# Kernel tuning notes

Measured on AMD Instinct MI355X. Metric: run time of the kernel, lower is better.

The kernel has to match this reference:

```python
import jax, jax.numpy as jnp
import numpy as np

N_NODES = 100000
N_EDGES = 3200000
N_GRAPHS = 64


def gcn_conv(x, W, b, src, dst, n_nodes):
    # PyG GCNConv: add self-loops, symmetric degree normalization, then
    # out[dst] += norm * (x @ W)[src], plus bias.
    h = x @ W  # [N, out]
    loop = jnp.arange(n_nodes)
    s = jnp.concatenate([src, loop])
    d = jnp.concatenate([dst, loop])
    deg = jax.ops.segment_sum(jnp.ones_like(d, dtype=h.dtype), d, num_segments=n_nodes)
    dinv = jnp.where(deg > 0, jax.lax.rsqrt(deg), 0.0)
    norm = dinv[s] * dinv[d]  # [E+N]
    msg = norm[:, None] * h[s]  # gather + scale
    out = jax.ops.segment_sum(msg, d, num_segments=n_nodes)  # scatter-add
    return out + b


def global_mean_pool(x, batch, num_graphs):
    sums = jax.ops.segment_sum(x, batch, num_segments=num_graphs)
    cnts = jax.ops.segment_sum(jnp.ones((x.shape[0],), x.dtype), batch, num_segments=num_graphs)
    return sums / jnp.maximum(cnts, 1.0)[:, None]


def setup_inputs() -> dict:
    key = jax.random.key(0)
    ks = jax.random.split(key, 12)
    x = jax.random.normal(ks[0], (N_NODES, 128), dtype=jnp.float32)
    edge_index = jax.random.randint(ks[1], (2, N_EDGES), 0, N_NODES, dtype=jnp.int64 if jax.config.jax_enable_x64 else jnp.int32)
    batch = jnp.sort(jax.random.randint(ks[2], (N_NODES,), 0, N_GRAPHS))
    def lin(k, fan_in, fan_out):
        bound = 1.0 / np.sqrt(fan_in)
        kw, kb = jax.random.split(k)
        W = jax.random.uniform(kw, (fan_in, fan_out), minval=-bound, maxval=bound, dtype=jnp.float32)
        b = jax.random.uniform(kb, (fan_out,), minval=-bound, maxval=bound, dtype=jnp.float32)
        return W, b
    W1, b1 = lin(ks[3], 128, 16)
    W2, b2 = lin(ks[4], 16, 32)
    Wf1, bf1 = lin(ks[5], 32, 64)
    Wf2, bf2 = lin(ks[6], 64, 8)
    return {"x": x, "edge_index": edge_index, "batch": batch,
            "W1": W1, "b1": b1, "W2": W2, "b2": b2,
            "Wf1": Wf1, "bf1": bf1, "Wf2": Wf2, "bf2": bf2}


def reference(x, edge_index, batch, W1, b1, W2, b2, Wf1, bf1, Wf2, bf2):
    src, dst = edge_index[0], edge_index[1]
    n = x.shape[0]
    h = jax.nn.relu(gcn_conv(x, W1, b1, src, dst, n))
    h = jax.nn.relu(gcn_conv(h, W2, b2, src, dst, n))
    g = global_mean_pool(h, batch, N_GRAPHS)  # [G, 32]
    g = jax.nn.relu(g @ Wf1 + bf1)
    return g @ Wf2 + bf2  # [G, num_actions]
```

## Files before the change

### kernel.cpp

```cpp
#include <hip/hip_runtime.h>
#include <hip/hip_fp16.h>

#define N_NODES  100000
#define N_EDGES  3200000
#define N_GRAPHS 64

#define BSHIFT   7
#define BMASK    127
#define NBUCK    782
#define CAP      4608
#define PB_BLK   1000
#define PB_CHUNK 3200
#define PB_CH4   800

#define SCALE1   2097152.0f
#define ISCALE1  (1.0f / 2097152.0f)
#define SCALE2   1048576.0f
#define ISCALE2  (1.0f / 1048576.0f)
#define SCALEP   65536.0f
#define ISCALEP  (1.0f / 65536.0f)


#define EDGEACC(p_, r_, SC) { \
    int d_ = (int)((p_) >> 17); \
    float2 f01_ = __half22float2(*(const __half2*)&(r_).x); \
    float2 f23_ = __half22float2(*(const __half2*)&(r_).y); \
    int* a_ = &acc[d_ * 17 + f4 * 4]; \
    atomicAdd(a_ + 0, __float2int_rn(f01_.x * (SC))); \
    atomicAdd(a_ + 1, __float2int_rn(f01_.y * (SC))); \
    atomicAdd(a_ + 2, __float2int_rn(f23_.x * (SC))); \
    atomicAdd(a_ + 3, __float2int_rn(f23_.y * (SC))); }

#define LOADR(k_, w_, P_) uint2 r##k_ = *(const uint2*)((P_) + ((w_) & 0x1FFFF) * 16 + f4 * 4);

__global__ void __launch_bounds__(256) hist_pass(const int* __restrict__ dst,
                                                 unsigned int* __restrict__ histG) {
    __shared__ int hist[NBUCK];
    int t = threadIdx.x;
    const int4* d4p = (const int4*)(dst + blockIdx.x * PB_CHUNK);
    for (int i = t; i < NBUCK; i += 256) hist[i] = 0;
    __syncthreads();
    int i = t;
    for (; i + 256 < PB_CH4; i += 512) {
        int4 a = d4p[i];
        int4 b = d4p[i + 256];
        atomicAdd(&hist[a.x >> BSHIFT], 1); atomicAdd(&hist[a.y >> BSHIFT], 1);
        atomicAdd(&hist[a.z >> BSHIFT], 1); atomicAdd(&hist[a.w >> BSHIFT], 1);
        atomicAdd(&hist[b.x >> BSHIFT], 1); atomicAdd(&hist[b.y >> BSHIFT], 1);
        atomicAdd(&hist[b.z >> BSHIFT], 1); atomicAdd(&hist[b.w >> BSHIFT], 1);
    }
    for (; i < PB_CH4; i += 256) {
        int4 a = d4p[i];
        atomicAdd(&hist[a.x >> BSHIFT], 1); atomicAdd(&hist[a.y >> BSHIFT], 1);
        atomicAdd(&hist[a.z >> BSHIFT], 1); atomicAdd(&hist[a.w >> BSHIFT], 1);
    }
    __syncthreads();
    for (int i2 = t; i2 < NBUCK; i2 += 256)
        histG[blockIdx.x * NBUCK + i2] = (unsigned int)hist[i2];
}

__global__ void __launch_bounds__(256) scan_pass(const unsigned int* __restrict__ histG,
                                                 unsigned int* __restrict__ baseG,
                                                 int* __restrict__ cntG) {
    __shared__ unsigned int s[256];
    int b = blockIdx.x, t = threadIdx.x;
    unsigned int v0 = (t * 4 + 0 < PB_BLK) ? histG[(t * 4 + 0) * NBUCK + b] : 0;
    unsigned int v1 = (t * 4 + 1 < PB_BLK) ? histG[(t * 4 + 1) * NBUCK + b] : 0;
    unsigned int v2 = (t * 4 + 2 < PB_BLK) ? histG[(t * 4 + 2) * NBUCK + b] : 0;
    unsigned int v3 = (t * 4 + 3 < PB_BLK) ? histG[(t * 4 + 3) * NBUCK + b] : 0;
    unsigned int tot = v0 + v1 + v2 + v3;
    s[t] = tot;
    __syncthreads();
    for (int o = 1; o < 256; o <<= 1) {
        unsigned int x = (t >= o) ? s[t - o] : 0;
        __syncthreads();
        s[t] += x;
        __syncthreads();
    }
    unsigned int ex = s[t] - tot;
    unsigned int base = (unsigned int)b * CAP + ex;
    if (t * 4 + 0 < PB_BLK) baseG[b * PB_BLK + t * 4 + 0] = base;
    if (t * 4 + 1 < PB_BLK) baseG[b * PB_BLK + t * 4 + 1] = base + v0;
    if (t * 4 + 2 < PB_BLK) baseG[b * PB_BLK + t * 4 + 2] = base + v0 + v1;
    if (t * 4 + 3 < PB_BLK) baseG[b * PB_BLK + t * 4 + 3] = base + v0 + v1 + v2;
    if (t == 255) cntG[b] = (int)(ex + tot);
}

#define PLACE1(d_, s_) { \
    int bb_ = (d_) >> BSHIFT; \
    unsigned int pk_ = ((unsigned int)((d_) & BMASK) << 17) | (unsigned int)(s_); \
    int slot_ = atomicAdd(&cur[bb_], 1); \
    st[slot_] = pk_; bkt[slot_] = (unsigned short)bb_; }

__global__ void __launch_bounds__(256) place_pass(const int* __restrict__ src,
                                                  const int* __restrict__ dst,
                                                  const unsigned int* __restrict__ histG,
                                                  const unsigned int* __restrict__ baseG,
                                                  unsigned int* __restrict__ stage) {
    __shared__ int off[NBUCK];
    __shared__ int cur[NBUCK];
    __shared__ unsigned int gbase[NBUCK];
    __shared__ int part[256];
    __shared__ unsigned int st[PB_CHUNK];
    __shared__ unsigned short bkt[PB_CHUNK];
    int t = threadIdx.x, blk = blockIdx.x;

    int b4 = t * 4;
    int h0 = (b4 + 0 < NBUCK) ? (int)histG[blk * NBUCK + b4 + 0] : 0;
    int h1 = (b4 + 1 < NBUCK) ? (int)histG[blk * NBUCK + b4 + 1] : 0;
    int h2 = (b4 + 2 < NBUCK) ? (int)histG[blk * NBUCK + b4 + 2] : 0;
    int h3 = (b4 + 3 < NBUCK) ? (int)histG[blk * NBUCK + b4 + 3] : 0;
    int tot = h0 + h1 + h2 + h3;
    part[t] = tot;
    __syncthreads();
    for (int o = 1; o < 256; o <<= 1) {
        int v = (t >= o) ? part[t - o] : 0;
        __syncthreads();
        part[t] += v;
        __syncthreads();
    }
    int ex = part[t] - tot;
    if (b4 + 0 < NBUCK) { off[b4 + 0] = ex;                cur[b4 + 0] = ex; }
    if (b4 + 1 < NBUCK) { off[b4 + 1] = ex + h0;           cur[b4 + 1] = ex + h0; }
    if (b4 + 2 < NBUCK) { off[b4 + 2] = ex + h0 + h1;      cur[b4 + 2] = ex + h0 + h1; }
    if (b4 + 3 < NBUCK) { off[b4 + 3] = ex + h0 + h1 + h2; cur[b4 + 3] = ex + h0 + h1 + h2; }
    for (int i = t; i < NBUCK; i += 256) gbase[i] = baseG[i * PB_BLK + blk];
    __syncthreads();

    const int4* d4p = (const int4*)(dst + blk * PB_CHUNK);
    const int4* s4p = (const int4*)(src + blk * PB_CHUNK);
    int i = t;
    for (; i + 256 < PB_CH4; i += 512) {
        int4 d0 = d4p[i],        s0 = s4p[i];
        int4 d1_ = d4p[i + 256], s1_ = s4p[i + 256];
        PLACE1(d0.x, s0.x); PLACE1(d0.y, s0.y); PLACE1(d0.z, s0.z); PLACE1(d0.w, s0.w);
        PLACE1(d1_.x, s1_.x); PLACE1(d1_.y, s1_.y); PLACE1(d1_.z, s1_.z); PLACE1(d1_.w, s1_.w);
    }
    for (; i < PB_CH4; i += 256) {
        int4 d0 = d4p[i], s0 = s4p[i];
        PLACE1(d0.x, s0.x); PLACE1(d0.y, s0.y); PLACE1(d0.z, s0.z); PLACE1(d0.w, s0.w);
    }
    __syncthreads();

    for (int i2 = t; i2 < PB_CHUNK; i2 += 256) {
        int b = bkt[i2];
        unsigned int gs = gbase[b] + (unsigned int)(i2 - off[b]);
        if (gs < (unsigned int)(b + 1) * CAP) stage[gs] = st[i2];
    }
}

__global__ void __launch_bounds__(256) bucket_dinv(const unsigned int* __restrict__ stage,
                                                   const int* __restrict__ cntG,
                                                   float* __restrict__ dinv) {
    __shared__ int ldeg[128];
    int b = blockIdx.x, t = threadIdx.x;
    int base = b * CAP;
    int cnt = cntG[b]; if (cnt > CAP) cnt = CAP;
    if (t < 128) ldeg[t] = 0;
    __syncthreads();
    int i0 = t * 4;
    for (; i0 + 4 <= cnt; i0 += 1024) {
        uint4 p = *(const uint4*)(stage + base + i0);
        atomicAdd(&ldeg[p.x >> 17], 1);
        atomicAdd(&ldeg[p.y >> 17], 1);
        atomicAdd(&ldeg[p.z >> 17], 1);
        atomicAdd(&ldeg[p.w >> 17], 1);
    }
    for (int j = i0; j < cnt && j < i0 + 4; j++)
        atomicAdd(&ldeg[stage[base + j] >> 17], 1);
    __syncthreads();
    int v = b * 128 + t;
    if (t < 128 && v < N_NODES) dinv[v] = rsqrtf((float)(ldeg[t] + 1));
}

#define MM1_ROWS 64
__global__ void __launch_bounds__(256) mm1(const float* __restrict__ x,
                                           const float* __restrict__ W,
                                           const float* __restrict__ dinv,
                                           __half* __restrict__ hs) {
    __shared__ float ws[128 * 16];
    __shared__ float xs[MM1_ROWS * 132];
    int t = threadIdx.x;
    int row0 = blockIdx.x * MM1_ROWS;
    for (int i = t; i < 2048; i += 256) ws[i] = W[i];
    for (int i = t; i < 2048; i += 256) {
        int r = i >> 5, c4 = (i & 31) * 4;
        int v = row0 + r;
        float4 val = (v < N_NODES) ? *(const float4*)(x + (size_t)v * 128 + c4)
                                   : make_float4(0.f, 0.f, 0.f, 0.f);
        *(float4*)&xs[r * 132 + c4] = val;
    }
    __syncthreads();
    int row = t >> 2, c4 = (t & 3) * 4;
    int v = row0 + row;
    if (v < N_NODES) {
        float dv = dinv[v];
        float a0 = 0.f, a1 = 0.f, a2 = 0.f, a3 = 0.f;
#pragma unroll
        for (int k = 0; k < 128; k++) {
            float xv = xs[row * 132 + k];
            float4 w4 = *(const float4*)&ws[k * 16 + c4];
            a0 += xv * w4.x; a1 += xv * w4.y; a2 += xv * w4.z; a3 += xv * w4.w;
        }
        __half2 h01 = __floats2half2_rn(a0 * dv, a1 * dv);
        __half2 h23 = __floats2half2_rn(a2 * dv, a3 * dv);
        uint2 o = make_uint2(*(unsigned*)&h01, *(unsigned*)&h23);
        *(uint2*)(hs + (size_t)v * 16 + c4) = o;
    }
}

__global__ void __launch_bounds__(256) gather1(const unsigned int* __restrict__ stage,
                                               const int* __restrict__ cntG,
                                               const __half* __restrict__ hs,
                                               const float* __restrict__ dinv,
                                               const float* __restrict__ b1,
                                               __half* __restrict__ d1) {
    __shared__ int acc[128 * 17];
    int b = blockIdx.x, t = threadIdx.x;
    int base = b * CAP;
    int cnt = cntG[b]; if (cnt > CAP) cnt = CAP;
    for (int i = t; i < 128 * 17; i += 256) acc[i] = 0;
    __syncthreads();
    int f4 = t & 3;
    int q = t >> 2;
    int i0 = q * 16;
    for (; i0 + 16 <= cnt; i0 += 1024) {
        const uint4* sp = (const uint4*)(stage + base + i0);
        uint4 pa = sp[0], pb = sp[1], pc = sp[2], pd = sp[3];
        LOADR(0,  pa.x, hs) LOADR(1,  pa.y, hs) LOADR(2,  pa.z, hs) LOADR(3,  pa.w, hs)
        LOADR(4,  pb.x, hs) LOADR(5,  pb.y, hs) LOADR(6,  pb.z, hs) LOADR(7,  pb.w, hs)
        LOADR(8,  pc.x, hs) LOADR(9,  pc.y, hs) LOADR(10, pc.z, hs) LOADR(11, pc.w, hs)
        LOADR(12, pd.x, hs) LOADR(13, pd.y, hs) LOADR(14, pd.z, hs) LOADR(15, pd.w, hs)
        EDGEACC(pa.x, r0,  SCALE1) EDGEACC(pa.y, r1,  SCALE1)
        EDGEACC(pa.z, r2,  SCALE1) EDGEACC(pa.w, r3,  SCALE1)
        EDGEACC(pb.x, r4,  SCALE1) EDGEACC(pb.y, r5,  SCALE1)
        EDGEACC(pb.z, r6,  SCALE1) EDGEACC(pb.w, r7,  SCALE1)
        EDGEACC(pc.x, r8,  SCALE1) EDGEACC(pc.y, r9,  SCALE1)
        EDGEACC(pc.z, r10, SCALE1) EDGEACC(pc.w, r11, SCALE1)
        EDGEACC(pd.x, r12, SCALE1) EDGEACC(pd.y, r13, SCALE1)
        EDGEACC(pd.z, r14, SCALE1) EDGEACC(pd.w, r15, SCALE1)
    }
    for (int j = i0; j < cnt && j < i0 + 16; j++) {
        unsigned int p = stage[base + j];
        uint2 r = *(const uint2*)(hs + (p & 0x1FFFF) * 16 + f4 * 4);
        EDGEACC(p, r, SCALE1);
    }
    __syncthreads();
    for (int i = t; i < 512; i += 256) {
        int n = i >> 2, kq = (i & 3) * 4, v = b * 128 + n;
        if (v < N_NODES) {
            float dv = dinv[v];
            const int* ar = &acc[n * 17 + kq];
            uint2 sh = *(const uint2*)(hs + (size_t)v * 16 + kq);
            float2 s01 = __half22float2(*(const __half2*)&sh.x);
            float2 s23 = __half22float2(*(const __half2*)&sh.y);
            float r0 = dv * ((float)ar[0] * ISCALE1 + s01.x) + b1[kq + 0];
            float r1 = dv * ((float)ar[1] * ISCALE1 + s01.y) + b1[kq + 1];
            float r2 = dv * ((float)ar[2] * ISCALE1 + s23.x) + b1[kq + 2];
            float r3 = dv * ((float)ar[3] * ISCALE1 + s23.y) + b1[kq + 3];
            __half2 h01 = __floats2half2_rn(r0 > 0.f ? dv * r0 : 0.f,
                                            r1 > 0.f ? dv * r1 : 0.f);
            __half2 h23 = __floats2half2_rn(r2 > 0.f ? dv * r2 : 0.f,
                                            r3 > 0.f ? dv * r3 : 0.f);
            uint2 o = make_uint2(*(unsigned*)&h01, *(unsigned*)&h23);
            *(uint2*)(d1 + (size_t)v * 16 + kq) = o;
        }
    }
}

__global__ void __launch_bounds__(256) gather2(const unsigned int* __restrict__ stage,
                                               const int* __restrict__ cntG,
                                               const __half* __restrict__ d1,
                                               const float* __restrict__ dinv,
                                               const float* __restrict__ W2,
                                               const float* __restrict__ b2,
                                               const int* __restrict__ batch,
                                               float* __restrict__ gsum,
                                               float* __restrict__ gcnt) {
    __shared__ int acc[128 * 17];
    __shared__ float wl[512];
    __shared__ int lsum[N_GRAPHS * 32];
    __shared__ int lcnt[N_GRAPHS];
    __shared__ int lbat[128];
    float* accf = (float*)acc;
    int b = blockIdx.x, t = threadIdx.x;
    int base = b * CAP;
    int cnt = cntG[b]; if (cnt > CAP) cnt = CAP;
    for (int i = t; i < 128 * 17; i += 256) acc[i] = 0;
    for (int i = t; i < 512; i += 256) wl[i] = W2[i];
    for (int i = t; i < N_GRAPHS * 32; i += 256) lsum[i] = 0;
    if (t < N_GRAPHS) lcnt[t] = 0;
    if (t < 128) {
        int v = b * 128 + t;
        lbat[t] = (v < N_NODES) ? batch[v] : 0;
    }
    __syncthreads();
    int f4 = t & 3;
    int q = t >> 2;
    int i0 = q * 16;
    for (; i0 + 16 <= cnt; i0 += 1024) {
        const uint4* sp = (const uint4*)(stage + base + i0);
        uint4 pa = sp[0], pb = sp[1], pc = sp[2], pd = sp[3];
        LOADR(0,  pa.x, d1) LOADR(1,  pa.y, d1) LOADR(2,  pa.z, d1) LOADR(3,  pa.w, d1)
        LOADR(4,  pb.x, d1) LOADR(5,  pb.y, d1) LOADR(6,  pb.z, d1) LOADR(7,  pb.w, d1)
        LOADR(8,  pc.x, d1) LOADR(9,  pc.y, d1) LOADR(10, pc.z, d1) LOADR(11, pc.w, d1)
        LOADR(12, pd.x, d1) LOADR(13, pd.y, d1) LOADR(14, pd.z, d1) LOADR(15, pd.w, d1)
        EDGEACC(pa.x, r0,  SCALE2) EDGEACC(pa.y, r1,  SCALE2)
        EDGEACC(pa.z, r2,  SCALE2) EDGEACC(pa.w, r3,  SCALE2)
        EDGEACC(pb.x, r4,  SCALE2) EDGEACC(pb.y, r5,  SCALE2)
        EDGEACC(pb.z, r6,  SCALE2) EDGEACC(pb.w, r7,  SCALE2)
        EDGEACC(pc.x, r8,  SCALE2) EDGEACC(pc.y, r9,  SCALE2)
        EDGEACC(pc.z, r10, SCALE2) EDGEACC(pc.w, r11, SCALE2)
        EDGEACC(pd.x, r12, SCALE2) EDGEACC(pd.y, r13, SCALE2)
        EDGEACC(pd.z, r14, SCALE2) EDGEACC(pd.w, r15, SCALE2)
    }
    for (int j = i0; j < cnt && j < i0 + 16; j++) {
        unsigned int p = stage[base + j];
        uint2 r = *(const uint2*)(d1 + (p & 0x1FFFF) * 16 + f4 * 4);
        EDGEACC(p, r, SCALE2);
    }
    __syncthreads();
    for (int i = t; i < 2048; i += 256) {
        int n = i >> 4, k = i & 15, v = b * 128 + n;
        float sum = (float)acc[n * 17 + k] * ISCALE2;
        if (v < N_NODES) sum += __half2float(d1[v * 16 + k]);
        accf[n * 17 + k] = sum;
    }
    __syncthreads();
    int k = t & 31, l0 = t >> 5;
    for (int g = 0; g < 16; g++) {
        int n = l0 + g * 8, v = b * 128 + n;
        if (v < N_NODES) {
            const float* ar = &accf[n * 17];
            float a = 0.f;
#pragma unroll
            for (int j = 0; j < 16; j++) a += ar[j] * wl[j * 32 + k];
            float r = dinv[v] * a + b2[k];
            r = r > 0.f ? r : 0.f;
            int gg = lbat[n];
            atomicAdd(&lsum[gg * 32 + k], __float2int_rn(r * SCALEP));
            if (k == 0) atomicAdd(&lcnt[gg], 1);
        }
    }
    __syncthreads();
    int last = 127; if (b * 128 + last > N_NODES - 1) last = N_NODES - 1 - b * 128;
    int gmin = lbat[0], gmax = lbat[last];
    int ng = gmax - gmin + 1;
    for (int i = t; i < ng * 32; i += 256) {
        int gg = gmin + (i >> 5);
        int iv = lsum[gg * 32 + (i & 31)];
        if (iv != 0) atomicAdd(&gsum[gg * 32 + (i & 31)], (float)iv * ISCALEP);
    }
    for (int i = t; i < ng; i += 256) {
        int iv = lcnt[gmin + i];
        if (iv != 0) atomicAdd(&gcnt[gmin + i], (float)iv);
    }
}

__global__ void head(const float* __restrict__ gsum, const float* __restrict__ gcnt,
                     const float* __restrict__ Wf1, const float* __restrict__ bf1,
                     const float* __restrict__ Wf2, const float* __restrict__ bf2,
                     float* __restrict__ out) {
    __shared__ float gm[64 * 32];
    __shared__ float f1[64 * 64];
    int t = threadIdx.x;
    for (int i = t; i < 2048; i += 1024) {
        int g = i >> 5;
        float c = gcnt[g]; if (c < 1.f) c = 1.f;
        gm[i] = gsum[i] / c;
    }
    __syncthreads();
    for (int i = t; i < 4096; i += 1024) {
        int r = i >> 6, c = i & 63;
        float a = bf1[c];
#pragma unroll
        for (int j = 0; j < 32; j++) a += gm[r * 32 + j] * Wf1[j * 64 + c];
        f1[i] = a > 0.f ? a : 0.f;
    }
    __syncthreads();
    if (t < 512) {
        int r = t >> 3, c = t & 7;
        float a = bf2[c];
#pragma unroll
        for (int j = 0; j < 64; j++) a += f1[r * 64 + j] * Wf2[j * 8 + c];
        out[t] = a;
    }
}

extern "C" void kernel_launch(void* const* d_in, const int* in_sizes, int n_in,
                              void* d_out, int out_size, void* d_ws, size_t ws_size,
                              hipStream_t stream) {
    const float* x   = (const float*)d_in[0];
    const int*   ei  = (const int*)d_in[1];
    const int*   bat = (const int*)d_in[2];
    const float* W1  = (const float*)d_in[3];
    const float* b1  = (const float*)d_in[4];
    const float* W2  = (const float*)d_in[5];
    const float* b2  = (const float*)d_in[6];
    const float* Wf1 = (const float*)d_in[7];
    const float* bf1 = (const float*)d_in[8];
    const float* Wf2 = (const float*)d_in[9];
    const float* bf2 = (const float*)d_in[10];
    const int* src = ei;
    const int* dst = ei + N_EDGES;
    float* out = (float*)d_out;

    char* ws = (char*)d_ws;
    unsigned int* histG = (unsigned int*)(ws + 0);
    unsigned int* baseG = (unsigned int*)(ws + 3128000);
    int*          cntG  = (int*)         (ws + 6256000);
    unsigned int* stage = (unsigned int*)(ws + 6260224);
    float*        dinv  = (float*)       (ws + 20674048);
    float*        gsum  = (float*)       (ws + 21074048);
    float*        gcnt  = (float*)       (ws + 21082240);
    __half*       hs1   = (__half*)      (ws + 21082496);
    __half*       d1    = (__half*)      (ws + 24282496);

    hipMemsetAsync(gsum, 0, (N_GRAPHS * 32 + N_GRAPHS) * sizeof(float), stream);

    hist_pass<<<PB_BLK, 256, 0, stream>>>(dst, histG);
    scan_pass<<<NBUCK, 256, 0, stream>>>(histG, baseG, cntG);
    place_pass<<<PB_BLK, 256, 0, stream>>>(src, dst, histG, baseG, stage);
    bucket_dinv<<<NBUCK, 256, 0, stream>>>(stage, cntG, dinv);

    mm1<<<(N_NODES + MM1_ROWS - 1) / MM1_ROWS, 256, 0, stream>>>(x, W1, dinv, hs1);
    gather1<<<NBUCK, 256, 0, stream>>>(stage, cntG, hs1, dinv, b1, d1);

    gather2<<<NBUCK, 256, 0, stream>>>(stage, cntG, d1, dinv, W2, b2, bat, gsum, gcnt);

    head<<<1, 1024, 0, stream>>>(gsum, gcnt, Wf1, bf1, Wf2, bf2, out);
}
```

Baseline: 235.0 us.

## Sort bucketed edges by destination into CSR and gather without atomics

```diff
diff --git a/kernel.cpp b/kernel.cpp
--- a/kernel.cpp
+++ b/kernel.cpp
@@ -13,25 +13,9 @@
 #define PB_CHUNK 3200
 #define PB_CH4   800
 
-#define SCALE1   2097152.0f
-#define ISCALE1  (1.0f / 2097152.0f)
-#define SCALE2   1048576.0f
-#define ISCALE2  (1.0f / 1048576.0f)
 #define SCALEP   65536.0f
 #define ISCALEP  (1.0f / 65536.0f)
 
-
-#define EDGEACC(p_, r_, SC) { \
-    int d_ = (int)((p_) >> 17); \
-    float2 f01_ = __half22float2(*(const __half2*)&(r_).x); \
-    float2 f23_ = __half22float2(*(const __half2*)&(r_).y); \
-    int* a_ = &acc[d_ * 17 + f4 * 4]; \
-    atomicAdd(a_ + 0, __float2int_rn(f01_.x * (SC))); \
-    atomicAdd(a_ + 1, __float2int_rn(f01_.y * (SC))); \
-    atomicAdd(a_ + 2, __float2int_rn(f23_.x * (SC))); \
-    atomicAdd(a_ + 3, __float2int_rn(f23_.y * (SC))); }
-
-#define LOADR(k_, w_, P_) uint2 r##k_ = *(const uint2*)((P_) + ((w_) & 0x1FFFF) * 16 + f4 * 4);
 
 __global__ void __launch_bounds__(256) hist_pass(const int* __restrict__ dst,
                                                  unsigned int* __restrict__ histG) {
@@ -149,10 +133,14 @@
     }
 }
 
-__global__ void __launch_bounds__(256) bucket_dinv(const unsigned int* __restrict__ stage,
-                                                   const int* __restrict__ cntG,
-                                                   float* __restrict__ dinv) {
+__global__ void __launch_bounds__(256) sort_pass(unsigned int* __restrict__ stage,
+                                                 const int* __restrict__ cntG,
+                                                 int* __restrict__ noffG,
+                                                 float* __restrict__ dinv) {
     __shared__ int ldeg[128];
+    __shared__ int scn[128];
+    __shared__ int cur[128];
+    __shared__ unsigned int sorted[CAP];
     int b = blockIdx.x, t = threadIdx.x;
     int base = b * CAP;
     int cnt = cntG[b]; if (cnt > CAP) cnt = CAP;
@@ -169,8 +157,38 @@
     for (int j = i0; j < cnt && j < i0 + 4; j++)
         atomicAdd(&ldeg[stage[base + j] >> 17], 1);
     __syncthreads();
-    int v = b * 128 + t;
-    if (t < 128 && v < N_NODES) dinv[v] = rsqrtf((float)(ldeg[t] + 1));
+    if (t < 128) scn[t] = ldeg[t];
+    __syncthreads();
+    for (int o = 1; o < 128; o <<= 1) {
+        int v = (t < 128 && t >= o) ? scn[t - o] : 0;
+        __syncthreads();
+        if (t < 128) scn[t] += v;
+        __syncthreads();
+    }
+    if (t < 128) {
+        int start = scn[t] - ldeg[t];
+        cur[t] = start;
+        noffG[b * 129 + t] = base + start;
+        int v = b * 128 + t;
+        if (v < N_NODES) dinv[v] = rsqrtf((float)(ldeg[t] + 1));
+    }
+    if (t == 0) noffG[b * 129 + 128] = base + cnt;
+    __syncthreads();
+    i0 = t * 4;
+    for (; i0 + 4 <= cnt; i0 += 1024) {
+        uint4 p = *(const uint4*)(stage + base + i0);
+        sorted[atomicAdd(&cur[p.x >> 17], 1)] = p.x;
+        sorted[atomicAdd(&cur[p.y >> 17], 1)] = p.y;
+        sorted[atomicAdd(&cur[p.z >> 17], 1)] = p.z;
+        sorted[atomicAdd(&cur[p.w >> 17], 1)] = p.w;
+    }
+    for (int j = i0; j < cnt && j < i0 + 4; j++) {
+        unsigned int p = stage[base + j];
+        sorted[atomicAdd(&cur[p >> 17], 1)] = p;
+    }
+    __syncthreads();
+    for (int i = t; i < cnt; i += 256)
+        stage[base + i] = sorted[i];
 }
 
 #define MM1_ROWS 64
@@ -209,67 +227,62 @@
     }
 }
 
+#define GADD1(p_) { \
+    uint2 r_ = *(const uint2*)(TBL + ((p_) & 0x1FFFF) * 16 + f4 * 4); \
+    float2 x_ = __half22float2(*(const __half2*)&r_.x); \
+    float2 y_ = __half22float2(*(const __half2*)&r_.y); \
+    a0 += x_.x; a1 += x_.y; a2 += y_.x; a3 += y_.y; }
+
+#define GLOOP() \
+    int i = off; \
+    for (; i + 8 <= end; i += 8) { \
+        unsigned p0 = stage[i+0], p1 = stage[i+1], p2 = stage[i+2], p3 = stage[i+3]; \
+        unsigned p4 = stage[i+4], p5 = stage[i+5], p6 = stage[i+6], p7 = stage[i+7]; \
+        GADD1(p0) GADD1(p1) GADD1(p2) GADD1(p3) \
+        GADD1(p4) GADD1(p5) GADD1(p6) GADD1(p7) \
+    } \
+    for (; i < end; i++) { unsigned p_ = stage[i]; GADD1(p_) }
+
 __global__ void __launch_bounds__(256) gather1(const unsigned int* __restrict__ stage,
-                                               const int* __restrict__ cntG,
+                                               const int* __restrict__ noffG,
                                                const __half* __restrict__ hs,
                                                const float* __restrict__ dinv,
                                                const float* __restrict__ b1,
                                                __half* __restrict__ d1) {
-    __shared__ int acc[128 * 17];
     int b = blockIdx.x, t = threadIdx.x;
-    int base = b * CAP;
-    int cnt = cntG[b]; if (cnt > CAP) cnt = CAP;
-    for (int i = t; i < 128 * 17; i += 256) acc[i] = 0;
-    __syncthreads();
     int f4 = t & 3;
     int q = t >> 2;
-    int i0 = q * 16;
-    for (; i0 + 16 <= cnt; i0 += 1024) {
-        const uint4* sp = (const uint4*)(stage + base + i0);
-        uint4 pa = sp[0], pb = sp[1], pc = sp[2], pd = sp[3];
-        LOADR(0,  pa.x, hs) LOADR(1,  pa.y, hs) LOADR(2,  pa.z, hs) LOADR(3,  pa.w, hs)
-        LOADR(4,  pb.x, hs) LOADR(5,  pb.y, hs) LOADR(6,  pb.z, hs) LOADR(7,  pb.w, hs)
-        LOADR(8,  pc.x, hs) LOADR(9,  pc.y, hs) LOADR(10, pc.z, hs) LOADR(11, pc.w, hs)
-        LOADR(12, pd.x, hs) LOADR(13, pd.y, hs) LOADR(14, pd.z, hs) LOADR(15, pd.w, hs)
-        EDGEACC(pa.x, r0,  SCALE1) EDGEACC(pa.y, r1,  SCALE1)
-        EDGEACC(pa.z, r2,  SCALE1) EDGEACC(pa.w, r3,  SCALE1)
-        EDGEACC(pb.x, r4,  SCALE1) EDGEACC(pb.y, r5,  SCALE1)
-        EDGEACC(pb.z, r6,  SCALE1) EDGEACC(pb.w, r7,  SCALE1)
-        EDGEACC(pc.x, r8,  SCALE1) EDGEACC(pc.y, r9,  SCALE1)
-        EDGEACC(pc.z, r10, SCALE1) EDGEACC(pc.w, r11, SCALE1)
-        EDGEACC(pd.x, r12, SCALE1) EDGEACC(pd.y, r13, SCALE1)
-        EDGEACC(pd.z, r14, SCALE1) EDGEACC(pd.w, r15, SCALE1)
-    }
-    for (int j = i0; j < cnt && j < i0 + 16; j++) {
-        unsigned int p = stage[base + j];
-        uint2 r = *(const uint2*)(hs + (p & 0x1FFFF) * 16 + f4 * 4);
-        EDGEACC(p, r, SCALE1);
-    }
-    __syncthreads();
-    for (int i = t; i < 512; i += 256) {
-        int n = i >> 2, kq = (i & 3) * 4, v = b * 128 + n;
+    const __half* TBL = hs;
+    float4 bb = *(const float4*)(b1 + f4 * 4);
+#pragma unroll
+    for (int h = 0; h < 2; h++) {
+        int n = q + h * 64;
+        int v = b * 128 + n;
+        int off = noffG[b * 129 + n];
+        int end = noffG[b * 129 + n + 1];
+        float a0 = 0.f, a1 = 0.f, a2 = 0.f, a3 = 0.f;
+        GLOOP()
         if (v < N_NODES) {
             float dv = dinv[v];
-            const int* ar = &acc[n * 17 + kq];
-            uint2 sh = *(const uint2*)(hs + (size_t)v * 16 + kq);
+            uint2 sh = *(const uint2*)(hs + (size_t)v * 16 + f4 * 4);
             float2 s01 = __half22float2(*(const __half2*)&sh.x);
             float2 s23 = __half22float2(*(const __half2*)&sh.y);
-            float r0 = dv * ((float)ar[0] * ISCALE1 + s01.x) + b1[kq + 0];
-            float r1 = dv * ((float)ar[1] * ISCALE1 + s01.y) + b1[kq + 1];
-            float r2 = dv * ((float)ar[2] * ISCALE1 + s23.x) + b1[kq + 2];
-            float r3 = dv * ((float)ar[3] * ISCALE1 + s23.y) + b1[kq + 3];
+            float r0 = dv * (a0 + s01.x) + bb.x;
+            float r1 = dv * (a1 + s01.y) + bb.y;
+            float r2 = dv * (a2 + s23.x) + bb.z;
+            float r3 = dv * (a3 + s23.y) + bb.w;
             __half2 h01 = __floats2half2_rn(r0 > 0.f ? dv * r0 : 0.f,
                                             r1 > 0.f ? dv * r1 : 0.f);
             __half2 h23 = __floats2half2_rn(r2 > 0.f ? dv * r2 : 0.f,
                                             r3 > 0.f ? dv * r3 : 0.f);
             uint2 o = make_uint2(*(unsigned*)&h01, *(unsigned*)&h23);
-            *(uint2*)(d1 + (size_t)v * 16 + kq) = o;
+            *(uint2*)(d1 + (size_t)v * 16 + f4 * 4) = o;
         }
     }
 }
 
 __global__ void __launch_bounds__(256) gather2(const unsigned int* __restrict__ stage,
-                                               const int* __restrict__ cntG,
+                                               const int* __restrict__ noffG,
                                                const __half* __restrict__ d1,
                                                const float* __restrict__ dinv,
                                                const float* __restrict__ W2,
@@ -277,16 +290,15 @@
                                                const int* __restrict__ batch,
                                                float* __restrict__ gsum,
                                                float* __restrict__ gcnt) {
-    __shared__ int acc[128 * 17];
+    __shared__ float accf[128 * 17];
     __shared__ float wl[512];
     __shared__ int lsum[N_GRAPHS * 32];
     __shared__ int lcnt[N_GRAPHS];
     __shared__ int lbat[128];
-    float* accf = (float*)acc;
     int b = blockIdx.x, t = threadIdx.x;
-    int base = b * CAP;
-    int cnt = cntG[b]; if (cnt > CAP) cnt = CAP;
-    for (int i = t; i < 128 * 17; i += 256) acc[i] = 0;
+    int f4 = t & 3;
+    int q = t >> 2;
+    const __half* TBL = d1;
     for (int i = t; i < 512; i += 256) wl[i] = W2[i];
     for (int i = t; i < N_GRAPHS * 32; i += 256) lsum[i] = 0;
     if (t < N_GRAPHS) lcnt[t] = 0;
@@ -294,37 +306,23 @@
         int v = b * 128 + t;
         lbat[t] = (v < N_NODES) ? batch[v] : 0;
     }
-    __syncthreads();
-    int f4 = t & 3;
-    int q = t >> 2;
-    int i0 = q * 16;
-    for (; i0 + 16 <= cnt; i0 += 1024) {
-        const uint4* sp = (const uint4*)(stage + base + i0);
-        uint4 pa = sp[0], pb = sp[1], pc = sp[2], pd = sp[3];
-        LOADR(0,  pa.x, d1) LOADR(1,  pa.y, d1) LOADR(2,  pa.z, d1) LOADR(3,  pa.w, d1)
-        LOADR(4,  pb.x, d1) LOADR(5,  pb.y, d1) LOADR(6,  pb.z, d1) LOADR(7,  pb.w, d1)
-        LOADR(8,  pc.x, d1) LOADR(9,  pc.y, d1) LOADR(10, pc.z, d1) LOADR(11, pc.w, d1)
-        LOADR(12, pd.x, d1) LOADR(13, pd.y, d1) LOADR(14, pd.z, d1) LOADR(15, pd.w, d1)
-        EDGEACC(pa.x, r0,  SCALE2) EDGEACC(pa.y, r1,  SCALE2)
-        EDGEACC(pa.z, r2,  SCALE2) EDGEACC(pa.w, r3,  SCALE2)
-        EDGEACC(pb.x, r4,  SCALE2) EDGEACC(pb.y, r5,  SCALE2)
-        EDGEACC(pb.z, r6,  SCALE2) EDGEACC(pb.w, r7,  SCALE2)
-        EDGEACC(pc.x, r8,  SCALE2) EDGEACC(pc.y, r9,  SCALE2)
-        EDGEACC(pc.z, r10, SCALE2) EDGEACC(pc.w, r11, SCALE2)
-        EDGEACC(pd.x, r12, SCALE2) EDGEACC(pd.y, r13, SCALE2)
-        EDGEACC(pd.z, r14, SCALE2) EDGEACC(pd.w, r15, SCALE2)
-    }
-    for (int j = i0; j < cnt && j < i0 + 16; j++) {
-        unsigned int p = stage[base + j];
-        uint2 r = *(const uint2*)(d1 + (p & 0x1FFFF) * 16 + f4 * 4);
-        EDGEACC(p, r, SCALE2);
-    }
-    __syncthreads();
-    for (int i = t; i < 2048; i += 256) {
-        int n = i >> 4, k = i & 15, v = b * 128 + n;
-        float sum = (float)acc[n * 17 + k] * ISCALE2;
-        if (v < N_NODES) sum += __half2float(d1[v * 16 + k]);
-        accf[n * 17 + k] = sum;
+#pragma unroll
+    for (int h = 0; h < 2; h++) {
+        int n = q + h * 64;
+        int v = b * 128 + n;
+        int off = noffG[b * 129 + n];
+        int end = noffG[b * 129 + n + 1];
+        float a0 = 0.f, a1 = 0.f, a2 = 0.f, a3 = 0.f;
+        GLOOP()
+        float s0 = 0.f, s1 = 0.f, s2 = 0.f, s3 = 0.f;
+        if (v < N_NODES) {
+            uint2 sh = *(const uint2*)(d1 + (size_t)v * 16 + f4 * 4);
+            float2 s01 = __half22float2(*(const __half2*)&sh.x);
+            float2 s23 = __half22float2(*(const __half2*)&sh.y);
+            s0 = s01.x; s1 = s01.y; s2 = s23.x; s3 = s23.y;
+        }
+        float* ap = &accf[n * 17 + f4 * 4];
+        ap[0] = a0 + s0; ap[1] = a1 + s1; ap[2] = a2 + s2; ap[3] = a3 + s3;
     }
     __syncthreads();
     int k = t & 31, l0 = t >> 5;
@@ -413,20 +411,21 @@
     float*        dinv  = (float*)       (ws + 20674048);
     float*        gsum  = (float*)       (ws + 21074048);
     float*        gcnt  = (float*)       (ws + 21082240);
-    __half*       hs1   = (__half*)      (ws + 21082496);
-    __half*       d1    = (__half*)      (ws + 24282496);
+    int*          noffG = (int*)         (ws + 21082496);
+    __half*       hs1   = (__half*)      (ws + 21486080);
+    __half*       d1    = (__half*)      (ws + 24686080);
 
     hipMemsetAsync(gsum, 0, (N_GRAPHS * 32 + N_GRAPHS) * sizeof(float), stream);
 
     hist_pass<<<PB_BLK, 256, 0, stream>>>(dst, histG);
     scan_pass<<<NBUCK, 256, 0, stream>>>(histG, baseG, cntG);
     place_pass<<<PB_BLK, 256, 0, stream>>>(src, dst, histG, baseG, stage);
-    bucket_dinv<<<NBUCK, 256, 0, stream>>>(stage, cntG, dinv);
+    sort_pass<<<NBUCK, 256, 0, stream>>>(stage, cntG, noffG, dinv);
 
     mm1<<<(N_NODES + MM1_ROWS - 1) / MM1_ROWS, 256, 0, stream>>>(x, W1, dinv, hs1);
-    gather1<<<NBUCK, 256, 0, stream>>>(stage, cntG, hs1, dinv, b1, d1);
-
-    gather2<<<NBUCK, 256, 0, stream>>>(stage, cntG, d1, dinv, W2, b2, bat, gsum, gcnt);
+    gather1<<<NBUCK, 256, 0, stream>>>(stage, noffG, hs1, dinv, b1, d1);
+
+    gather2<<<NBUCK, 256, 0, stream>>>(stage, noffG, d1, dinv, W2, b2, bat, gsum, gcnt);
 
     head<<<1, 1024, 0, stream>>>(gsum, gcnt, Wf1, bf1, Wf2, bf2, out);
 }
```

Result: slower. 242.3 us (+3.1%).
